# Optimization experiments

Hardware: AMD Instinct MI355X
Metric: run time of the kernel (lower is better)

## Reference

```python
import jax, jax.numpy as jnp
import numpy as np

K_DIM = 1024
N_HEADS = 16
HEAD = K_DIM // N_HEADS


def setup_inputs() -> dict:
    key = jax.random.key(0)
    kx, kq, kk, kv, ko = jax.random.split(key, 5)
    b, t = 2, 2048
    scale = 1.0 / np.sqrt(K_DIM)
    x = jax.random.normal(kx, (b, t, K_DIM), dtype=jnp.float32)
    # nn.Linear(k, k, bias=False): y = x @ W.T, W has shape [k, k]
    Wq = jax.random.normal(kq, (K_DIM, K_DIM), dtype=jnp.float32) * scale
    Wk = jax.random.normal(kk, (K_DIM, K_DIM), dtype=jnp.float32) * scale
    Wv = jax.random.normal(kv, (K_DIM, K_DIM), dtype=jnp.float32) * scale
    Wo = jax.random.normal(ko, (K_DIM, K_DIM), dtype=jnp.float32) * scale
    return {"x": x, "Wq": Wq, "Wk": Wk, "Wv": Wv, "Wo": Wo}


def reference(x, Wq, Wk, Wv, Wo):
    b, t, k = x.shape
    h, hs = N_HEADS, HEAD
    # projections (torch Linear: x @ W.T), split heads -> [b, h, t, hs]
    Q = (x @ Wq.T).reshape(b, t, h, hs).transpose(0, 2, 1, 3)
    Kt = (x @ Wk.T).reshape(b, t, h, hs).transpose(0, 2, 1, 3)
    V = (x @ Wv.T).reshape(b, t, h, hs).transpose(0, 2, 1, 3)
    # NOTE: original scales by sqrt(k) (model dim), not sqrt(head_size)
    scores = jnp.einsum('bhqd,bhkd->bhqk', Q, Kt) / jnp.sqrt(jnp.asarray(k, x.dtype))
    W = jax.nn.softmax(scores, axis=-1)
    O = jnp.einsum('bhqk,bhkd->bhqd', W, V)  # [b, h, t, hs]
    O = O.transpose(0, 2, 1, 3).reshape(b, t, k)
    return O @ Wo.T
```

## Files before the change

kernel.cpp:

```cpp
#include <hip/hip_runtime.h>
#include <hip/hip_bf16.h>

#define N_HEADS 16
#define HEAD 64
#define B_SZ 2
#define T_SZ 2048
#define KD 1024
#define M_TOT (B_SZ * T_SZ)

typedef short bf16x8 __attribute__((ext_vector_type(8)));
typedef short bf16x4 __attribute__((ext_vector_type(4)));
typedef float f32x4  __attribute__((ext_vector_type(4)));

#define MFMA32(a, b, c) __builtin_amdgcn_mfma_f32_16x16x32_bf16((a), (b), (c), 0, 0, 0)

__device__ __forceinline__ ushort f2bf(float f) {
    __hip_bfloat16 h = __float2bfloat16(f);
    return *reinterpret_cast<ushort*>(&h);
}

__device__ __forceinline__ ushort f2bf_fast(float f) {
    return (ushort)((__float_as_uint(f) + 0x8000u) >> 16);
}

__device__ __forceinline__ float exp2fast(float x) {
#if __has_builtin(__builtin_amdgcn_exp2f)
    return __builtin_amdgcn_exp2f(x);
#else
    return exp2f(x);
#endif
}

__device__ __forceinline__ void gl2lds16(const ushort* g, void* l) {
    __builtin_amdgcn_global_load_lds(
        (const __attribute__((address_space(1))) unsigned int*)g,
        (__attribute__((address_space(3))) unsigned int*)l, 16, 0, 0);
}

#define RAW_BARRIER() do { asm volatile("" ::: "memory"); \
                           __builtin_amdgcn_s_barrier();  \
                           asm volatile("" ::: "memory"); } while (0)

__global__ void cvt_all(const float* __restrict__ x,
                        const float* __restrict__ Wq, const float* __restrict__ Wk,
                        const float* __restrict__ Wv, const float* __restrict__ Wo,
                        ushort* __restrict__ xb, ushort* __restrict__ wb) {
    const int NX = (M_TOT * KD) / 4;
    const int NW = (KD * KD) / 4;
    int i = blockIdx.x * blockDim.x + threadIdx.x;
    float4 v;
    ushort* dst;
    if (i < NX) {
        v = reinterpret_cast<const float4*>(x)[i];
        dst = xb + (size_t)i * 4;
    } else {
        int j = i - NX;
        int w = j >> 18;
        int r = j & (NW - 1);
        const float* s = (w == 0) ? Wq : (w == 1) ? Wk : (w == 2) ? Wv : Wo;
        v = reinterpret_cast<const float4*>(s)[r];
        dst = wb + (size_t)w * KD * KD + (size_t)r * 4;
    }
    ushort4 o;
    o.x = f2bf(v.x); o.y = f2bf(v.y); o.z = f2bf(v.z); o.w = f2bf(v.w);
    *reinterpret_cast<ushort4*>(dst) = o;
}

__global__ __launch_bounds__(256) void gemm_qkv(const ushort* __restrict__ A,
                                                const ushort* __restrict__ Bm,
                                                ushort* __restrict__ Qbase) {
    const int bm = blockIdx.x;
    const int bn = blockIdx.y;
    __shared__ alignas(128) char As[2][16384];
    __shared__ alignas(128) char Bs[2][16384];
    const int tid = threadIdx.x;
    const int lane = tid & 63;
    const int w = tid >> 6;
    const int wr = w >> 1, wc = w & 1;
    const int r15 = lane & 15, q4 = lane >> 4;
    const int sl8 = lane >> 3;
    const int scol = (((lane & 7) * 16) ^ (sl8 << 4)) >> 1;

    f32x4 acc[4][4] = {};

    #define GSTAGE(buf, k0)                                                          \
        {                                                                            \
            _Pragma("unroll")                                                        \
            for (int rr = 0; rr < 4; ++rr) {                                         \
                int r = rr * 32 + w * 8 + sl8;                                       \
                gl2lds16(A  + (size_t)(bm * 128 + r) * 1024 + (k0) + scol,           \
                         &As[buf][(rr * 32 + w * 8) * 128]);                         \
                gl2lds16(Bm + (size_t)(bn * 128 + r) * 1024 + (k0) + scol,           \
                         &Bs[buf][(rr * 32 + w * 8) * 128]);                         \
            }                                                                        \
        }

    GSTAGE(0, 0);
    int cur = 0;
    for (int t = 0; t < 16; ++t) {
        GSTAGE(cur ^ 1, ((t + 1) & 15) * 64);
        asm volatile("s_waitcnt vmcnt(8)" ::: "memory");
        RAW_BARRIER();

        #pragma unroll
        for (int kk = 0; kk < 2; ++kk) {
            bf16x8 af[4], bfr[4];
            #pragma unroll
            for (int m = 0; m < 4; ++m) {
                int row = wr * 64 + m * 16 + r15;
                af[m] = *(const bf16x8*)(&As[cur][row * 128 + ((kk * 64 + q4 * 16) ^ ((row & 7) << 4))]);
            }
            #pragma unroll
            for (int n = 0; n < 4; ++n) {
                int row = wc * 64 + n * 16 + r15;
                bfr[n] = *(const bf16x8*)(&Bs[cur][row * 128 + ((kk * 64 + q4 * 16) ^ ((row & 7) << 4))]);
            }
            #pragma unroll
            for (int m = 0; m < 4; ++m)
                #pragma unroll
                for (int n = 0; n < 4; ++n)
                    acc[m][n] = MFMA32(af[m], bfr[n], acc[m][n]);
        }
        RAW_BARRIER();
        cur ^= 1;
    }
    #undef GSTAGE
    asm volatile("s_waitcnt vmcnt(0)" ::: "memory");
    RAW_BARRIER();

    const size_t seg = (size_t)32 * 2048 * 64;
    const int which = bn >> 3;
    const int row0 = bm * 128 + wr * 64;
    const int col0w = bn * 128 + wc * 64;

    if (which == 2) {
        #pragma unroll
        for (int m = 0; m < 4; ++m)
            #pragma unroll
            for (int n = 0; n < 4; ++n) {
                int col = col0w + n * 16 + r15;
                int rem = col & 1023;
                int head = rem >> 6;
                int d = rem & 63;
                int row_base = row0 + m * 16 + q4 * 4;
                int bidx = row_base >> 11;
                int t = row_base & 2047;
                int bh_ = bidx * 16 + head;
                int blk = (t >> 2) & 7;
                int npos = (blk < 4) ? (blk << 1) : ((blk << 1) - 7);
                int tp = (t & ~31) | (npos << 2);
                ushort4 o;
                o.x = f2bf(acc[m][n][0]); o.y = f2bf(acc[m][n][1]);
                o.z = f2bf(acc[m][n][2]); o.w = f2bf(acc[m][n][3]);
                *(ushort4*)(&Qbase[2 * seg + ((size_t)bh_ * 64 + d) * 2048 + tp]) = o;
            }
    } else {
        const float sc = (which == 0) ? 0.045084439f : 1.0f;
        char* ep = (char*)As + w * 8192;
        #pragma unroll
        for (int m = 0; m < 4; ++m)
            #pragma unroll
            for (int n = 0; n < 4; ++n)
                #pragma unroll
                for (int i = 0; i < 4; ++i) {
                    int row = m * 16 + q4 * 4 + i;
                    int dby = (n * 16 + r15) * 2;
                    *(ushort*)(ep + row * 128 + (dby ^ ((row & 7) << 4))) =
                        f2bf(acc[m][n][i] * sc);
                }
        const int head = (col0w & 1023) >> 6;
        #pragma unroll
        for (int j = 0; j < 8; ++j) {
            int row = (lane >> 3) + j * 8;
            bf16x8 vv = *(const bf16x8*)(ep + row * 128 +
                                         (((lane & 7) * 16) ^ ((row & 7) << 4)));
            int grow = row0 + row;
            int bidx = grow >> 11;
            int t = grow & 2047;
            *(bf16x8*)(&Qbase[(size_t)which * seg +
                              (((size_t)(bidx * 16 + head) * 2048 + t) * 64) + (lane & 7) * 8]) = vv;
        }
    }
}

__global__ __launch_bounds__(256) void gemm_o(const ushort* __restrict__ A,
                                              const ushort* __restrict__ Bm,
                                              float* __restrict__ C) {
    const int bm = blockIdx.x;
    const int bn = blockIdx.y;
    __shared__ alignas(128) char As[2][16384];
    __shared__ alignas(128) char Bs[2][8192];
    const int tid = threadIdx.x;
    const int lane = tid & 63;
    const int w = tid >> 6;
    const int wr = w >> 1, wc = w & 1;
    const int r15 = lane & 15, q4 = lane >> 4;
    const int sl8 = lane >> 3;
    const int scol = (((lane & 7) * 16) ^ (sl8 << 4)) >> 1;

    f32x4 acc[4][2] = {};

    #define OSTAGE(buf, k0)                                                          \
        {                                                                            \
            _Pragma("unroll")                                                        \
            for (int rr = 0; rr < 4; ++rr) {                                         \
                int r = w * 32 + rr * 8 + sl8;                                       \
                gl2lds16(A + (size_t)(bm * 128 + r) * 1024 + (k0) + scol,            \
                         &As[buf][(w * 32 + rr * 8) * 128]);                         \
            }                                                                        \
            _Pragma("unroll")                                                        \
            for (int rr = 0; rr < 2; ++rr) {                                         \
                int r = w * 16 + rr * 8 + sl8;                                       \
                gl2lds16(Bm + (size_t)(bn * 64 + r) * 1024 + (k0) + scol,            \
                         &Bs[buf][(w * 16 + rr * 8) * 128]);                         \
            }                                                                        \
        }

    OSTAGE(0, 0);
    int cur = 0;
    for (int t = 0; t < 16; ++t) {
        OSTAGE(cur ^ 1, ((t + 1) & 15) * 64);
        asm volatile("s_waitcnt vmcnt(6)" ::: "memory");
        RAW_BARRIER();

        #pragma unroll
        for (int kk = 0; kk < 2; ++kk) {
            bf16x8 af[4], bfr[2];
            #pragma unroll
            for (int m = 0; m < 4; ++m) {
                int row = wr * 64 + m * 16 + r15;
                af[m] = *(const bf16x8*)(&As[cur][row * 128 + ((kk * 64 + q4 * 16) ^ ((row & 7) << 4))]);
            }
            #pragma unroll
            for (int n = 0; n < 2; ++n) {
                int row = wc * 32 + n * 16 + r15;
                bfr[n] = *(const bf16x8*)(&Bs[cur][row * 128 + ((kk * 64 + q4 * 16) ^ ((row & 7) << 4))]);
            }
            #pragma unroll
            for (int m = 0; m < 4; ++m)
                #pragma unroll
                for (int n = 0; n < 2; ++n)
                    acc[m][n] = MFMA32(af[m], bfr[n], acc[m][n]);
        }
        RAW_BARRIER();
        cur ^= 1;
    }
    #undef OSTAGE
    asm volatile("s_waitcnt vmcnt(0)" ::: "memory");

    const int row0 = bm * 128 + wr * 64;
    const int col0 = bn * 64 + wc * 32;
    #pragma unroll
    for (int m = 0; m < 4; ++m)
        #pragma unroll
        for (int n = 0; n < 2; ++n)
            #pragma unroll
            for (int i = 0; i < 4; ++i)
                C[(size_t)(row0 + m * 16 + q4 * 4 + i) * 1024 + col0 + n * 16 + r15] =
                    acc[m][n][i];
}

__global__ __launch_bounds__(1024) void attn_fwd(const ushort* __restrict__ Qh,
                                                 const ushort* __restrict__ Kh,
                                                 const ushort* __restrict__ Vt,
                                                 ushort* __restrict__ Ob) {
    const int bh = blockIdx.x;
    const int qt = blockIdx.y;
    const int tid = threadIdx.x;
    const int lane = tid & 63, w = tid >> 6;
    const int grp = w >> 3, wl = w & 7;
    const int r15 = lane & 15, q4 = lane >> 4;

    const ushort* Qp = Qh + (size_t)bh * T_SZ * HEAD;
    const ushort* Kp = Kh + (size_t)bh * T_SZ * HEAD;
    const ushort* Vp = Vt + (size_t)bh * HEAD * T_SZ;

    __shared__ alignas(16) char SMEM[65536];
    char* Kbuf = SMEM + grp * 32768;
    char* Vbuf = Kbuf + 16384;

    const int srow = wl * 8 + (lane >> 3);
    const int sslot = (lane & 7) * 16;
    const int ssb = (sslot ^ ((srow & 7) << 4)) >> 1;
    const int kvbase = grp << 10;

    const int q0 = qt * 256 + wl * 32;
    bf16x8 qf[2][2];
    #pragma unroll
    for (int cc = 0; cc < 2; ++cc) {
        qf[cc][0] = *(const bf16x8*)(&Qp[(size_t)(q0 + cc * 16 + r15) * 64 + q4 * 8]);
        qf[cc][1] = *(const bf16x8*)(&Qp[(size_t)(q0 + cc * 16 + r15) * 64 + 32 + q4 * 8]);
    }

    const bf16x8 ones8 = {0x3F80, 0x3F80, 0x3F80, 0x3F80, 0x3F80, 0x3F80, 0x3F80, 0x3F80};

    f32x4 acc[2][4] = {};
    f32x4 acc_l[2] = {};

    #define STAGE(buf, kv0)                                                      \
        {                                                                        \
            gl2lds16(Kp + (size_t)(kvbase + (kv0) + srow) * 64 + ssb,            \
                     Kbuf + (buf) * 8192 + wl * 8 * 128);                        \
            gl2lds16(Vp + (size_t)srow * 2048 + kvbase + (kv0) + ssb,            \
                     Vbuf + (buf) * 8192 + wl * 8 * 128);                        \
        }

    STAGE(0, 0);
    int cur = 0;
    for (int it = 0; it < 16; ++it) {
        STAGE(cur ^ 1, ((it + 1) & 15) * 64);
        asm volatile("s_waitcnt vmcnt(2)" ::: "memory");
        RAW_BARRIER();

        const char* Ks = Kbuf + cur * 8192;
        const char* Vs = Vbuf + cur * 8192;

        bf16x8 kf[4][2];
        #pragma unroll
        for (int t4 = 0; t4 < 4; ++t4) {
            int row = t4 * 16 + r15;
            int sw = (row & 7) << 4;
            kf[t4][0] = *(const bf16x8*)(&Ks[row * 128 + ((q4 * 16) ^ sw)]);
            kf[t4][1] = *(const bf16x8*)(&Ks[row * 128 + ((64 + q4 * 16) ^ sw)]);
        }
        bf16x8 vf8[2][4];
        #pragma unroll
        for (int dt = 0; dt < 4; ++dt) {
            int row = dt * 16 + r15;
            int sw = (row & 7) << 4;
            #pragma unroll
            for (int t32 = 0; t32 < 2; ++t32)
                vf8[t32][dt] = *(const bf16x8*)(&Vs[row * 128 + ((t32 * 64 + q4 * 16) ^ sw)]);
        }

        f32x4 z[2][4];
        #pragma unroll
        for (int cc = 0; cc < 2; ++cc)
            #pragma unroll
            for (int t4 = 0; t4 < 4; ++t4) {
                f32x4 zz = {};
                zz = MFMA32(kf[t4][0], qf[cc][0], zz);
                zz = MFMA32(kf[t4][1], qf[cc][1], zz);
                z[cc][t4] = zz;
            }

        bf16x8 pb8[2][2];
        #pragma unroll
        for (int cc = 0; cc < 2; ++cc)
            #pragma unroll
            for (int t32 = 0; t32 < 2; ++t32)
                #pragma unroll
                for (int i = 0; i < 4; ++i) {
                    pb8[cc][t32][i]     = (short)f2bf_fast(exp2fast(z[cc][2 * t32][i]));
                    pb8[cc][t32][4 + i] = (short)f2bf_fast(exp2fast(z[cc][2 * t32 + 1][i]));
                }

        #pragma unroll
        for (int t32 = 0; t32 < 2; ++t32) {
            #pragma unroll
            for (int dt = 0; dt < 4; ++dt)
                #pragma unroll
                for (int cc = 0; cc < 2; ++cc)
                    acc[cc][dt] = MFMA32(vf8[t32][dt], pb8[cc][t32], acc[cc][dt]);
            #pragma unroll
            for (int cc = 0; cc < 2; ++cc)
                acc_l[cc] = MFMA32(ones8, pb8[cc][t32], acc_l[cc]);
        }

        RAW_BARRIER();
        cur ^= 1;
    }
    #undef STAGE

    asm volatile("s_waitcnt vmcnt(0)" ::: "memory");
    __syncthreads();

    float l0 = acc_l[0][0], l1 = acc_l[1][0];
    {
        float* MB = (float*)SMEM;
        #pragma unroll
        for (int rnd = 0; rnd < 2; ++rnd) {
            __syncthreads();
            if (grp == 1 && (wl >> 2) == rnd) {
                float* p = MB + (((wl & 3) * 64 + lane) * 34);
                #pragma unroll
                for (int cc = 0; cc < 2; ++cc)
                    #pragma unroll
                    for (int dt = 0; dt < 4; ++dt) {
                        *(float2*)(p + (cc * 4 + dt) * 4)     = make_float2(acc[cc][dt][0], acc[cc][dt][1]);
                        *(float2*)(p + (cc * 4 + dt) * 4 + 2) = make_float2(acc[cc][dt][2], acc[cc][dt][3]);
                    }
                *(float2*)(p + 32) = make_float2(l0, l1);
            }
            __syncthreads();
            if (grp == 0 && (wl >> 2) == rnd) {
                const float* p = MB + (((wl & 3) * 64 + lane) * 34);
                #pragma unroll
                for (int cc = 0; cc < 2; ++cc)
                    #pragma unroll
                    for (int dt = 0; dt < 4; ++dt)
                        #pragma unroll
                        for (int i = 0; i < 4; ++i)
                            acc[cc][dt][i] += p[(cc * 4 + dt) * 4 + i];
                l0 += p[32];
                l1 += p[33];
            }
        }
    }

    if (grp == 0) {
        const int b = bh >> 4, h = bh & 15;
        #pragma unroll
        for (int cc = 0; cc < 2; ++cc) {
            float inv = 1.0f / (cc ? l1 : l0);
            int q = q0 + cc * 16 + r15;
            #pragma unroll
            for (int dt = 0; dt < 4; ++dt) {
                ushort4 o;
                o.x = f2bf(acc[cc][dt][0] * inv);
                o.y = f2bf(acc[cc][dt][1] * inv);
                o.z = f2bf(acc[cc][dt][2] * inv);
                o.w = f2bf(acc[cc][dt][3] * inv);
                *(ushort4*)(&Ob[((size_t)(b * T_SZ + q)) * KD + h * HEAD + dt * 16 + q4 * 4]) = o;
            }
        }
    }
}

extern "C" void kernel_launch(void* const* d_in, const int* in_sizes, int n_in,
                              void* d_out, int out_size, void* d_ws, size_t ws_size,
                              hipStream_t stream) {
    const float* x  = (const float*)d_in[0];
    const float* Wq = (const float*)d_in[1];
    const float* Wk = (const float*)d_in[2];
    const float* Wv = (const float*)d_in[3];
    const float* Wo = (const float*)d_in[4];

    char* ws = (char*)d_ws;
    const size_t MB = 1024 * 1024;
    ushort* xb    = (ushort*)(ws + 0);
    ushort* Wqkvb = (ushort*)(ws + 8  * MB);
    ushort* Wob   = Wqkvb + 3 * (size_t)KD * KD;
    ushort* Qh    = (ushort*)(ws + 16 * MB);
    ushort* Kh    = (ushort*)(ws + 24 * MB);
    ushort* VhT   = (ushort*)(ws + 32 * MB);
    ushort* Ob    = (ushort*)(ws + 40 * MB);

    {
        int total4 = (M_TOT * KD) / 4 + KD * KD;
        cvt_all<<<total4 / 256, 256, 0, stream>>>(x, Wq, Wk, Wv, Wo, xb, Wqkvb);
    }

    gemm_qkv<<<dim3(32, 24), 256, 0, stream>>>(xb, Wqkvb, Qh);
    attn_fwd<<<dim3(32, 8), 1024, 0, stream>>>(Qh, Kh, VhT, Ob);
    gemm_o<<<dim3(32, 16), 256, 0, stream>>>(Ob, Wob, (float*)d_out);
}
```

Baseline: 105.0 us.

## Single-buffer GEMM LDS, remap blocks across XCDs, stage V-transpose stores via LDS

```diff
diff --git a/kernel.cpp b/kernel.cpp
--- a/kernel.cpp
+++ b/kernel.cpp
@@ -69,10 +69,12 @@
 __global__ __launch_bounds__(256) void gemm_qkv(const ushort* __restrict__ A,
                                                 const ushort* __restrict__ Bm,
                                                 ushort* __restrict__ Qbase) {
-    const int bm = blockIdx.x;
-    const int bn = blockIdx.y;
-    __shared__ alignas(128) char As[2][16384];
-    __shared__ alignas(128) char Bs[2][16384];
+    const int bid = blockIdx.x;
+    const int L = (bid & 7) * 96 + (bid >> 3);
+    const int bm = L & 31;
+    const int bn = L >> 5;
+    __shared__ alignas(128) char As[16384];
+    __shared__ alignas(128) char Bs[16384];
     const int tid = threadIdx.x;
     const int lane = tid & 63;
     const int w = tid >> 6;
@@ -83,23 +85,14 @@
 
     f32x4 acc[4][4] = {};
 
-    #define GSTAGE(buf, k0)                                                          \
-        {                                                                            \
-            _Pragma("unroll")                                                        \
-            for (int rr = 0; rr < 4; ++rr) {                                         \
-                int r = rr * 32 + w * 8 + sl8;                                       \
-                gl2lds16(A  + (size_t)(bm * 128 + r) * 1024 + (k0) + scol,           \
-                         &As[buf][(rr * 32 + w * 8) * 128]);                         \
-                gl2lds16(Bm + (size_t)(bn * 128 + r) * 1024 + (k0) + scol,           \
-                         &Bs[buf][(rr * 32 + w * 8) * 128]);                         \
-            }                                                                        \
-        }
-
-    GSTAGE(0, 0);
-    int cur = 0;
-    for (int t = 0; t < 16; ++t) {
-        GSTAGE(cur ^ 1, ((t + 1) & 15) * 64);
-        asm volatile("s_waitcnt vmcnt(8)" ::: "memory");
+    for (int k0 = 0; k0 < 1024; k0 += 64) {
+        #pragma unroll
+        for (int rr = 0; rr < 4; ++rr) {
+            int r = rr * 32 + w * 8 + sl8;
+            gl2lds16(A  + (size_t)(bm * 128 + r) * 1024 + k0 + scol, &As[(rr * 32 + w * 8) * 128]);
+            gl2lds16(Bm + (size_t)(bn * 128 + r) * 1024 + k0 + scol, &Bs[(rr * 32 + w * 8) * 128]);
+        }
+        asm volatile("s_waitcnt vmcnt(0)" ::: "memory");
         RAW_BARRIER();
 
         #pragma unroll
@@ -108,12 +101,12 @@
             #pragma unroll
             for (int m = 0; m < 4; ++m) {
                 int row = wr * 64 + m * 16 + r15;
-                af[m] = *(const bf16x8*)(&As[cur][row * 128 + ((kk * 64 + q4 * 16) ^ ((row & 7) << 4))]);
+                af[m] = *(const bf16x8*)(&As[row * 128 + ((kk * 64 + q4 * 16) ^ ((row & 7) << 4))]);
             }
             #pragma unroll
             for (int n = 0; n < 4; ++n) {
                 int row = wc * 64 + n * 16 + r15;
-                bfr[n] = *(const bf16x8*)(&Bs[cur][row * 128 + ((kk * 64 + q4 * 16) ^ ((row & 7) << 4))]);
+                bfr[n] = *(const bf16x8*)(&Bs[row * 128 + ((kk * 64 + q4 * 16) ^ ((row & 7) << 4))]);
             }
             #pragma unroll
             for (int m = 0; m < 4; ++m)
@@ -122,41 +115,42 @@
                     acc[m][n] = MFMA32(af[m], bfr[n], acc[m][n]);
         }
         RAW_BARRIER();
-        cur ^= 1;
-    }
-    #undef GSTAGE
-    asm volatile("s_waitcnt vmcnt(0)" ::: "memory");
-    RAW_BARRIER();
+    }
 
     const size_t seg = (size_t)32 * 2048 * 64;
     const int which = bn >> 3;
     const int row0 = bm * 128 + wr * 64;
     const int col0w = bn * 128 + wc * 64;
+    char* ep = ((w & 2) ? Bs : As) + (w & 1) * 8192;
 
     if (which == 2) {
         #pragma unroll
         for (int m = 0; m < 4; ++m)
             #pragma unroll
-            for (int n = 0; n < 4; ++n) {
-                int col = col0w + n * 16 + r15;
-                int rem = col & 1023;
-                int head = rem >> 6;
-                int d = rem & 63;
-                int row_base = row0 + m * 16 + q4 * 4;
-                int bidx = row_base >> 11;
-                int t = row_base & 2047;
-                int bh_ = bidx * 16 + head;
-                int blk = (t >> 2) & 7;
-                int npos = (blk < 4) ? (blk << 1) : ((blk << 1) - 7);
-                int tp = (t & ~31) | (npos << 2);
-                ushort4 o;
-                o.x = f2bf(acc[m][n][0]); o.y = f2bf(acc[m][n][1]);
-                o.z = f2bf(acc[m][n][2]); o.w = f2bf(acc[m][n][3]);
-                *(ushort4*)(&Qbase[2 * seg + ((size_t)bh_ * 64 + d) * 2048 + tp]) = o;
-            }
+            for (int n = 0; n < 4; ++n)
+                #pragma unroll
+                for (int i = 0; i < 4; ++i) {
+                    int dl = n * 16 + r15;
+                    int trow = m * 16 + q4 * 4 + i;
+                    int blk = (trow >> 2) & 7;
+                    int npos = (blk < 4) ? (blk << 1) : ((blk << 1) - 7);
+                    int tcol = (trow & 32) | (npos << 2) | (trow & 3);
+                    *(ushort*)(ep + dl * 128 + ((tcol * 2) ^ ((dl & 7) << 4))) =
+                        f2bf(acc[m][n][i]);
+                }
+        const int head = (col0w & 1023) >> 6;
+        const int bidx = row0 >> 11;
+        const int t0 = row0 & 2047;
+        #pragma unroll
+        for (int j = 0; j < 8; ++j) {
+            int d = (lane >> 3) + j * 8;
+            int c = lane & 7;
+            bf16x8 vv = *(const bf16x8*)(ep + d * 128 + ((c * 16) ^ ((d & 7) << 4)));
+            *(bf16x8*)(&Qbase[2 * seg + ((size_t)(bidx * 16 + head) * 64 + d) * 2048 +
+                              t0 + c * 8]) = vv;
+        }
     } else {
         const float sc = (which == 0) ? 0.045084439f : 1.0f;
-        char* ep = (char*)As + w * 8192;
         #pragma unroll
         for (int m = 0; m < 4; ++m)
             #pragma unroll
@@ -186,10 +180,12 @@
 __global__ __launch_bounds__(256) void gemm_o(const ushort* __restrict__ A,
                                               const ushort* __restrict__ Bm,
                                               float* __restrict__ C) {
-    const int bm = blockIdx.x;
-    const int bn = blockIdx.y;
-    __shared__ alignas(128) char As[2][16384];
-    __shared__ alignas(128) char Bs[2][8192];
+    const int bid = blockIdx.x;
+    const int L = (bid & 7) * 64 + (bid >> 3);
+    const int bm = L & 31;
+    const int bn = L >> 5;
+    __shared__ alignas(128) char As[16384];
+    __shared__ alignas(128) char Bs[8192];
     const int tid = threadIdx.x;
     const int lane = tid & 63;
     const int w = tid >> 6;
@@ -200,27 +196,18 @@
 
     f32x4 acc[4][2] = {};
 
-    #define OSTAGE(buf, k0)                                                          \
-        {                                                                            \
-            _Pragma("unroll")                                                        \
-            for (int rr = 0; rr < 4; ++rr) {                                         \
-                int r = w * 32 + rr * 8 + sl8;                                       \
-                gl2lds16(A + (size_t)(bm * 128 + r) * 1024 + (k0) + scol,            \
-                         &As[buf][(w * 32 + rr * 8) * 128]);                         \
-            }                                                                        \
-            _Pragma("unroll")                                                        \
-            for (int rr = 0; rr < 2; ++rr) {                                         \
-                int r = w * 16 + rr * 8 + sl8;                                       \
-                gl2lds16(Bm + (size_t)(bn * 64 + r) * 1024 + (k0) + scol,            \
-                         &Bs[buf][(w * 16 + rr * 8) * 128]);                         \
-            }                                                                        \
-        }
-
-    OSTAGE(0, 0);
-    int cur = 0;
-    for (int t = 0; t < 16; ++t) {
-        OSTAGE(cur ^ 1, ((t + 1) & 15) * 64);
-        asm volatile("s_waitcnt vmcnt(6)" ::: "memory");
+    for (int k0 = 0; k0 < 1024; k0 += 64) {
+        #pragma unroll
+        for (int rr = 0; rr < 4; ++rr) {
+            int r = w * 32 + rr * 8 + sl8;
+            gl2lds16(A + (size_t)(bm * 128 + r) * 1024 + k0 + scol, &As[(w * 32 + rr * 8) * 128]);
+        }
+        #pragma unroll
+        for (int rr = 0; rr < 2; ++rr) {
+            int r = w * 16 + rr * 8 + sl8;
+            gl2lds16(Bm + (size_t)(bn * 64 + r) * 1024 + k0 + scol, &Bs[(w * 16 + rr * 8) * 128]);
+        }
+        asm volatile("s_waitcnt vmcnt(0)" ::: "memory");
         RAW_BARRIER();
 
         #pragma unroll
@@ -229,12 +216,12 @@
             #pragma unroll
             for (int m = 0; m < 4; ++m) {
                 int row = wr * 64 + m * 16 + r15;
-                af[m] = *(const bf16x8*)(&As[cur][row * 128 + ((kk * 64 + q4 * 16) ^ ((row & 7) << 4))]);
+                af[m] = *(const bf16x8*)(&As[row * 128 + ((kk * 64 + q4 * 16) ^ ((row & 7) << 4))]);
             }
             #pragma unroll
             for (int n = 0; n < 2; ++n) {
                 int row = wc * 32 + n * 16 + r15;
-                bfr[n] = *(const bf16x8*)(&Bs[cur][row * 128 + ((kk * 64 + q4 * 16) ^ ((row & 7) << 4))]);
+                bfr[n] = *(const bf16x8*)(&Bs[row * 128 + ((kk * 64 + q4 * 16) ^ ((row & 7) << 4))]);
             }
             #pragma unroll
             for (int m = 0; m < 4; ++m)
@@ -243,10 +230,7 @@
                     acc[m][n] = MFMA32(af[m], bfr[n], acc[m][n]);
         }
         RAW_BARRIER();
-        cur ^= 1;
-    }
-    #undef OSTAGE
-    asm volatile("s_waitcnt vmcnt(0)" ::: "memory");
+    }
 
     const int row0 = bm * 128 + wr * 64;
     const int col0 = bn * 64 + wc * 32;
@@ -451,7 +435,7 @@
         cvt_all<<<total4 / 256, 256, 0, stream>>>(x, Wq, Wk, Wv, Wo, xb, Wqkvb);
     }
 
-    gemm_qkv<<<dim3(32, 24), 256, 0, stream>>>(xb, Wqkvb, Qh);
+    gemm_qkv<<<768, 256, 0, stream>>>(xb, Wqkvb, Qh);
     attn_fwd<<<dim3(32, 8), 1024, 0, stream>>>(Qh, Kh, VhT, Ob);
-    gemm_o<<<dim3(32, 16), 256, 0, stream>>>(Ob, Wob, (float*)d_out);
-}
+    gemm_o<<<512, 256, 0, stream>>>(Ob, Wob, (float*)d_out);
+}
```

After: 109.4 us. 4.2% more time.
